# Performance work log

Hardware: AMD Instinct MI355X
Metric: run time of the kernel (lower is better)

## Reference

```python
import jax, jax.numpy as jnp
import numpy as np

V, E, H, L, T, B = 50257, 1024, 16, 12, 128, 16
FF = 4 * E
STD = 0.02


def setup_inputs() -> dict:
    key = jax.random.key(0)
    ks = jax.random.split(key, 20)
    n = lambda k, shape: (jax.random.normal(k, shape, dtype=jnp.float32) * STD)
    inp = {
        'idx': jax.random.randint(ks[0], (B, T), 0, V, dtype=jnp.int64),
        'targets': jax.random.randint(ks[1], (B, T), 0, V, dtype=jnp.int64),
        'tok_emb': n(ks[2], (V, E)),
        'pos_emb': n(ks[3], (T, E)),
        'wq': n(ks[4], (L, E, E)),
        'wk': n(ks[5], (L, E, E)),
        'wv': n(ks[6], (L, E, E)),
        'w_proj': n(ks[7], (L, E, E)),
        'b_proj': jnp.zeros((L, E), jnp.float32),
        'ln1_g': jnp.ones((L, E), jnp.float32),
        'ln1_b': jnp.zeros((L, E), jnp.float32),
        'ln2_g': jnp.ones((L, E), jnp.float32),
        'ln2_b': jnp.zeros((L, E), jnp.float32),
        'w_fc1': n(ks[8], (L, E, FF)),
        'b_fc1': jnp.zeros((L, FF), jnp.float32),
        'w_fc2': n(ks[9], (L, FF, E)),
        'b_fc2': jnp.zeros((L, E), jnp.float32),
        'lnf_g': jnp.ones((E,), jnp.float32),
        'lnf_b': jnp.zeros((E,), jnp.float32),
        'w_head': n(ks[10], (E, V)),
        'b_head': jnp.zeros((V,), jnp.float32),
    }
    return inp


def _layernorm(x, g, b, eps=1e-5):
    m = x.mean(-1, keepdims=True)
    v = ((x - m) ** 2).mean(-1, keepdims=True)
    return (x - m) / jnp.sqrt(v + eps) * g + b


def _forward(idx, targets, tok_emb, pos_emb, wq, wk, wv, w_proj, b_proj,
             ln1_g, ln1_b, ln2_g, ln2_b, w_fc1, b_fc1, w_fc2, b_fc2,
             lnf_g, lnf_b, w_head, b_head):
    Bb, Tt = idx.shape
    x = tok_emb[idx] + pos_emb[:Tt]  # (B, T, E)
    causal = jnp.tril(jnp.ones((Tt, Tt), dtype=bool))
    scale = E ** (-0.5)  # NOTE: original scales by full n_embd, not head_size

    def block(x, p):
        (wq_l, wk_l, wv_l, wp_l, bp_l, g1, b1, g2, b2, wf1, bf1, wf2, bf2) = p
        h = _layernorm(x, g1, b1)
        q = (h @ wq_l).reshape(Bb, Tt, H, -1)
        k = (h @ wk_l).reshape(Bb, Tt, H, -1)
        v = (h @ wv_l).reshape(Bb, Tt, H, -1)
        sc = jnp.einsum('bthd,bshd->bhts', q, k) * scale
        sc = jnp.where(causal, sc, -jnp.inf)
        att = jax.nn.softmax(sc, axis=-1)
        o = jnp.einsum('bhts,bshd->bthd', att, v).reshape(Bb, Tt, E)
        x = x + o @ wp_l + bp_l
        h2 = _layernorm(x, g2, b2)
        x = x + jax.nn.relu(h2 @ wf1 + bf1) @ wf2 + bf2
        return x, None

    x, _ = jax.lax.scan(block, x, (wq, wk, wv, w_proj, b_proj, ln1_g, ln1_b,
                                   ln2_g, ln2_b, w_fc1, b_fc1, w_fc2, b_fc2))
    x = _layernorm(x, lnf_g, lnf_b)
    logits = x @ w_head + b_head  # (B, T, V)
    logp = jax.nn.log_softmax(logits, axis=-1)
    nll = -jnp.take_along_axis(logp.reshape(Bb * Tt, -1),
                               targets.reshape(-1, 1), axis=1)
    loss = nll.mean()
    return logits, loss


def reference(idx, targets, tok_emb, pos_emb, wq, wk, wv, w_proj, b_proj,
              ln1_g, ln1_b, ln2_g, ln2_b, w_fc1, b_fc1, w_fc2, b_fc2,
              lnf_g, lnf_b, w_head, b_head):
    return _forward(idx, targets, tok_emb, pos_emb, wq, wk, wv, w_proj, b_proj,
                    ln1_g, ln1_b, ln2_g, ln2_b, w_fc1, b_fc1, w_fc2, b_fc2,
                    lnf_g, lnf_b, w_head, b_head)
```

## Files before the change

kernel.cpp:

```cpp
#include <hip/hip_runtime.h>
#include <math.h>

typedef unsigned short u16;
typedef float f32x4 __attribute__((ext_vector_type(4)));
typedef short bf16x8 __attribute__((ext_vector_type(8)));
typedef unsigned short us4 __attribute__((ext_vector_type(4)));

#define DEVI __device__ __forceinline__

DEVI float bf2f(u16 u) { return __uint_as_float(((unsigned int)u) << 16); }
DEVI u16 f2bf(float f) {
    unsigned int u = __float_as_uint(f);
    u += 0x7fffu + ((u >> 16) & 1u);
    return (u16)(u >> 16);
}

__global__ __launch_bounds__(256) void k_embed(const int* __restrict__ idx,
                                               const float* __restrict__ te,
                                               const float* __restrict__ pe,
                                               float* __restrict__ x) {
    int m = blockIdx.x;
    int t = m & 127;
    int tok = idx[m];
    const f32x4* a = (const f32x4*)(te + (long)tok * 1024);
    const f32x4* p = (const f32x4*)(pe + (long)t * 1024);
    f32x4* o = (f32x4*)(x + (long)m * 1024);
    o[threadIdx.x] = a[threadIdx.x] + p[threadIdx.x];
}

DEVI void ln_body(f32x4 v, const float* g, const float* b, float* red,
                  int tid, int lane, int wid, u16* outrow) {
    float s = v.x + v.y + v.z + v.w;
#pragma unroll
    for (int o2 = 32; o2; o2 >>= 1) s += __shfl_xor(s, o2);
    if (lane == 0) red[wid] = s;
    __syncthreads();
    float mean = (red[0] + red[1] + red[2] + red[3]) * (1.0f / 1024.0f);
    f32x4 d; d.x = v.x - mean; d.y = v.y - mean; d.z = v.z - mean; d.w = v.w - mean;
    float sq = d.x * d.x + d.y * d.y + d.z * d.z + d.w * d.w;
#pragma unroll
    for (int o2 = 32; o2; o2 >>= 1) sq += __shfl_xor(sq, o2);
    if (lane == 0) red[4 + wid] = sq;
    __syncthreads();
    float rstd = rsqrtf((red[4] + red[5] + red[6] + red[7]) * (1.0f / 1024.0f) + 1e-5f);
    f32x4 gg = ((const f32x4*)g)[tid];
    f32x4 bb = ((const f32x4*)b)[tid];
    us4 o4;
    o4.x = f2bf(d.x * rstd * gg.x + bb.x);
    o4.y = f2bf(d.y * rstd * gg.y + bb.y);
    o4.z = f2bf(d.z * rstd * gg.z + bb.z);
    o4.w = f2bf(d.w * rstd * gg.w + bb.w);
    ((us4*)outrow)[tid] = o4;
}

__global__ __launch_bounds__(256) void k_ln(const float* __restrict__ x,
                                            const float* __restrict__ g,
                                            const float* __restrict__ b,
                                            u16* __restrict__ out) {
    __shared__ float red[8];
    int tid = threadIdx.x, lane = tid & 63, wid = tid >> 6;
    int r = blockIdx.x;
    f32x4 v = ((const f32x4*)(x + (long)r * 1024))[tid];
    ln_body(v, g, b, red, tid, lane, wid, out + (long)r * 1024);
}

__global__ __launch_bounds__(256) void k_comb_ln(float* __restrict__ x,
                                                 const float* __restrict__ p01,
                                                 const float* __restrict__ bias,
                                                 const float* __restrict__ g,
                                                 const float* __restrict__ b,
                                                 u16* __restrict__ out) {
    __shared__ float red[8];
    int tid = threadIdx.x, lane = tid & 63, wid = tid >> 6;
    int r = blockIdx.x;
    f32x4 v = ((const f32x4*)(x + (long)r * 1024))[tid];
    f32x4 p0 = ((const f32x4*)(p01 + (long)r * 1024))[tid];
    f32x4 p1 = ((const f32x4*)(p01 + 2048L * 1024 + (long)r * 1024))[tid];
    f32x4 bv = ((const f32x4*)bias)[tid];
    v.x += p0.x + p1.x + bv.x; v.y += p0.y + p1.y + bv.y;
    v.z += p0.z + p1.z + bv.z; v.w += p0.w + p1.w + bv.w;
    ((f32x4*)(x + (long)r * 1024))[tid] = v;
    ln_body(v, g, b, red, tid, lane, wid, out + (long)r * 1024);
}

DEVI void tr_tile(const float* __restrict__ in, u16* __restrict__ out,
                  int K, int N, int k0, int n0, int tid, float (*tile)[65]) {
    int trow = tid >> 4;
    int tcol = (tid & 15) * 4;
#pragma unroll
    for (int p = 0; p < 4; ++p) {
        int k = k0 + trow + p * 16;
        const float* src = in + (long)k * N + n0 + tcol;
#pragma unroll
        for (int j = 0; j < 4; ++j) {
            int n = n0 + tcol + j;
            tile[trow + p * 16][tcol + j] = (n < N) ? src[j] : 0.0f;
        }
    }
    __syncthreads();
#pragma unroll
    for (int p = 0; p < 4; ++p) {
        int n = n0 + trow + p * 16;
        if (n < N) {
            us4 o4;
#pragma unroll
            for (int j = 0; j < 4; ++j) o4[j] = f2bf(tile[tcol + j][trow + p * 16]);
            *(us4*)(out + (long)n * K + k0 + tcol) = o4;
        }
    }
}

__global__ __launch_bounds__(256) void k_tr_one(const float* __restrict__ in,
                                                u16* __restrict__ out, int K, int N) {
    __shared__ float tile[64][65];
    tr_tile(in, out, K, N, blockIdx.y * 64, blockIdx.x * 64, threadIdx.x, tile);
}

__global__ __launch_bounds__(256) void k_tr_layer(
    const float* __restrict__ wq, const float* __restrict__ wk,
    const float* __restrict__ wv, const float* __restrict__ wp,
    const float* __restrict__ f1, const float* __restrict__ f2,
    u16* __restrict__ oqkv, u16* __restrict__ oproj,
    u16* __restrict__ of1, u16* __restrict__ of2) {
    __shared__ float tile[64][65];
    int id = blockIdx.x;
    const float* in; u16* out; int K, N, txx, tyy;
    if (id < 1024) {
        int t = id >> 8, s2 = id & 255;
        txx = s2 & 15; tyy = s2 >> 4; K = 1024; N = 1024;
        in = (t == 0) ? wq : (t == 1) ? wk : (t == 2) ? wv : wp;
        out = (t == 3) ? oproj : oqkv + (long)t * 1024 * 1024;
    } else if (id < 2048) {
        int s2 = id - 1024;
        txx = s2 & 63; tyy = s2 >> 6; K = 1024; N = 4096; in = f1; out = of1;
    } else {
        int s2 = id - 2048;
        txx = s2 & 15; tyy = s2 >> 4; K = 4096; N = 1024; in = f2; out = of2;
    }
    tr_tile(in, out, K, N, tyy * 64, txx * 64, threadIdx.x, tile);
}

template <int ROWS>
DEVI void stage_tile(const u16* __restrict__ g, long row0, long rowmax, int ld,
                     int col0, char* lds, int tid) {
    constexpr int NCH = ROWS * 8;
#pragma unroll
    for (int p = 0; p < NCH / 256; ++p) {
        int c = tid + p * 256;
        int row = c >> 3;
        int gslot = c & 7;
        int gdata = gslot ^ (row & 7);
        long gr = row0 + row;
        if (gr > rowmax) gr = rowmax;
        const u16* src = g + gr * (long)ld + col0 + gdata * 8;
        char* dst = lds + ((long)((tid & 192) + p * 256)) * 16;
        __builtin_amdgcn_global_load_lds(
            (const __attribute__((address_space(1))) void*)src,
            (__attribute__((address_space(3))) void*)dst, 16, 0, 0);
    }
}

template <int ROWS>
DEVI void stage32(const u16* __restrict__ g, long row0, long rowmax, int ld,
                  int col0, char* lds, int tid) {
    constexpr int NP = ROWS * 4 / 512;
#pragma unroll
    for (int p = 0; p < NP; ++p) {
        int c = tid + p * 512;
        int row = c >> 2;
        int gslot = c & 3;
        int gdata = gslot ^ (row & 3) ^ ((row >> 2) & 3);
        long gr = row0 + row;
        if (gr > rowmax) gr = rowmax;
        const u16* src = g + gr * (long)ld + col0 + gdata * 8;
        char* dst = lds + ((long)((tid & 448) + p * 512)) * 16;
        __builtin_amdgcn_global_load_lds(
            (const __attribute__((address_space(1))) void*)src,
            (__attribute__((address_space(3))) void*)dst, 16, 0, 0);
    }
}

template <int BN, bool OUT_BF16, bool RELU, bool HAS_BIAS, bool HAS_RES, bool SPLITK>
__global__ __launch_bounds__(256, 2) void k_gemm(
    const u16* __restrict__ A, const u16* __restrict__ Bt,
    const float* __restrict__ bias, const float* __restrict__ res,
    float* __restrict__ Cf, u16* __restrict__ Cb,
    int M, int N, int K, int ldk, int ldc) {
    constexpr int NR = BN / 32;
    constexpr int ASZ = 128 * 64 * 2;
    constexpr int BSZ = BN * 64 * 2;
    __shared__ __align__(16) char lds[2 * (ASZ + BSZ)];
    int tid = threadIdx.x, lane = tid & 63, wid = tid >> 6;
    int l15 = lane & 15, l4 = lane >> 4;
    int wr = wid >> 1, wc = wid & 1;
    if constexpr (SPLITK) {
        int h = blockIdx.z;
        A += (long)h * K;
        Bt += (long)h * K;
        Cf += (long)h * M * (long)ldc;
    }
    long m0 = (long)blockIdx.y * 128;
    long n0 = (long)blockIdx.x * BN;
    f32x4 acc[4][NR] = {};
    const int nk = K >> 6;

    stage_tile<128>(A, m0, (long)M - 1, ldk, 0, lds, tid);
    stage_tile<BN>(Bt, n0, (long)N - 1, ldk, 0, lds + ASZ, tid);
    int cur = 0;
    for (int kt = 0; kt < nk; ++kt) {
        __syncthreads();
        if (kt + 1 < nk) {
            char* nb = lds + (cur ^ 1) * (ASZ + BSZ);
            stage_tile<128>(A, m0, (long)M - 1, ldk, (kt + 1) << 6, nb, tid);
            stage_tile<BN>(Bt, n0, (long)N - 1, ldk, (kt + 1) << 6, nb + ASZ, tid);
        }
        const char* ab = lds + cur * (ASZ + BSZ);
        const char* bb = ab + ASZ;
#pragma unroll
        for (int kh = 0; kh < 2; ++kh) {
            bf16x8 af[4], bfv[NR];
#pragma unroll
            for (int mi = 0; mi < 4; ++mi) {
                int row = wr * 64 + mi * 16 + l15;
                int slot = (kh * 4 + l4) ^ (row & 7);
                af[mi] = *(const bf16x8*)(ab + (row * 8 + slot) * 16);
            }
#pragma unroll
            for (int ni = 0; ni < NR; ++ni) {
                int row = wc * (BN / 2) + ni * 16 + l15;
                int slot = (kh * 4 + l4) ^ (row & 7);
                bfv[ni] = *(const bf16x8*)(bb + (row * 8 + slot) * 16);
            }
#pragma unroll
            for (int mi = 0; mi < 4; ++mi)
#pragma unroll
                for (int ni = 0; ni < NR; ++ni)
                    acc[mi][ni] = __builtin_amdgcn_mfma_f32_16x16x32_bf16(
                        af[mi], bfv[ni], acc[mi][ni], 0, 0, 0);
        }
        cur ^= 1;
    }
#pragma unroll
    for (int ni = 0; ni < NR; ++ni) {
        long n = n0 + wc * (BN / 2) + ni * 16 + l15;
        if (n < N) {
            float bv = HAS_BIAS ? bias[n] : 0.0f;
#pragma unroll
            for (int mi = 0; mi < 4; ++mi) {
#pragma unroll
                for (int j = 0; j < 4; ++j) {
                    long m = m0 + wr * 64 + mi * 16 + l4 * 4 + j;
                    float v = acc[mi][ni][j] + bv;
                    if (HAS_RES) v += res[m * (long)ldc + n];
                    if (RELU) v = fmaxf(v, 0.0f);
                    if (OUT_BF16) Cb[m * (long)ldc + n] = f2bf(v);
                    else Cf[m * (long)ldc + n] = v;
                }
            }
        }
    }
}

__global__ __launch_bounds__(512, 4) void k_head256(
    const u16* __restrict__ A, const u16* __restrict__ Bt,
    const float* __restrict__ bias, float* __restrict__ Cf,
    float2* __restrict__ part, int M, int N, int K, int ldc) {
    constexpr int ASZ = 256 * 32 * 2;
    constexpr int BSZ = 128 * 32 * 2;
    constexpr int TSZ = ASZ + BSZ;
    __shared__ __align__(16) char lds[128 * 129 * 4];
    int tid = threadIdx.x, lane = tid & 63, wid = tid >> 6;
    int l15 = lane & 15, l4 = lane >> 4;
    int wr = wid >> 1, wc = wid & 1;
    int bn = blockIdx.x, bm = blockIdx.y;
    long m0 = (long)bm * 256, n0 = (long)bn * 128;
    f32x4 acc[4][4] = {};
    const int nk = K >> 5;

    stage32<256>(A, m0, (long)M - 1, K, 0, lds, tid);
    stage32<128>(Bt, n0, (long)N - 1, K, 0, lds + ASZ, tid);
    int cur = 0;
    for (int kt = 0; kt < nk; ++kt) {
        __syncthreads();
        if (kt + 1 < nk) {
            char* nb = lds + (cur ^ 1) * TSZ;
            stage32<256>(A, m0, (long)M - 1, K, (kt + 1) << 5, nb, tid);
            stage32<128>(Bt, n0, (long)N - 1, K, (kt + 1) << 5, nb + ASZ, tid);
        }
        const char* ab = lds + cur * TSZ;
        const char* bb = ab + ASZ;
        bf16x8 af[4], bfv[4];
#pragma unroll
        for (int mi = 0; mi < 4; ++mi) {
            int row = wr * 64 + mi * 16 + l15;
            int slot = (l4 ^ (row & 3) ^ ((row >> 2) & 3)) & 3;
            af[mi] = *(const bf16x8*)(ab + (row * 4 + slot) * 16);
        }
#pragma unroll
        for (int ni = 0; ni < 4; ++ni) {
            int row = wc * 64 + ni * 16 + l15;
            int slot = (l4 ^ (row & 3) ^ ((row >> 2) & 3)) & 3;
            bfv[ni] = *(const bf16x8*)(bb + (row * 4 + slot) * 16);
        }
#pragma unroll
        for (int mi = 0; mi < 4; ++mi)
#pragma unroll
            for (int ni = 0; ni < 4; ++ni)
                acc[mi][ni] = __builtin_amdgcn_mfma_f32_16x16x32_bf16(
                    af[mi], bfv[ni], acc[mi][ni], 0, 0, 0);
        cur ^= 1;
    }
    const float BIG_NEG = -1e30f;
    float bvv[4];
#pragma unroll
    for (int ni = 0; ni < 4; ++ni) {
        long n = n0 + wc * 64 + ni * 16 + l15;
        bvv[ni] = (n < N) ? bias[n] : 0.0f;
    }
    float* ldsF = (float*)lds;
#pragma unroll
    for (int pass = 0; pass < 2; ++pass) {
        int rbase = pass * 128;
        __syncthreads();
        if ((wr >> 1) == pass) {
#pragma unroll
            for (int mi = 0; mi < 4; ++mi)
#pragma unroll
                for (int ni = 0; ni < 4; ++ni)
#pragma unroll
                    for (int j = 0; j < 4; ++j) {
                        int row = wr * 64 + mi * 16 + l4 * 4 + j - rbase;
                        int col = wc * 64 + ni * 16 + l15;
                        long n = n0 + col;
                        float v = acc[mi][ni][j] + bvv[ni];
                        if (n >= N) v = BIG_NEG;
                        ldsF[row * 129 + col] = v;
                    }
        }
        __syncthreads();
#pragma unroll 4
        for (int i = 0; i < 32; ++i) {
            int flat = tid + (i << 9);
            int row = flat >> 7, col = flat & 127;
            long n = n0 + col;
            if (n < N)
                __builtin_nontemporal_store(ldsF[row * 129 + col],
                                            &Cf[(m0 + rbase + row) * (long)ldc + n]);
        }
        if (tid < 256) {
            int r = tid >> 1, half = tid & 1;
            const float* rp = ldsF + r * 129 + half * 64;
            float mx = BIG_NEG;
#pragma unroll 8
            for (int c = 0; c < 64; ++c) mx = fmaxf(mx, rp[c]);
            float sm = 0.f;
#pragma unroll 8
            for (int c = 0; c < 64; ++c) sm += __expf(rp[c] - mx);
            float mo = __shfl_xor(mx, 1), so = __shfl_xor(sm, 1);
            float nm = fmaxf(mx, mo);
            float S = sm * __expf(mx - nm) + so * __expf(mo - nm);
            if (half == 0)
                part[(long)bn * M + m0 + rbase + r] = make_float2(nm, S);
        }
    }
}

__global__ __launch_bounds__(256) void k_attn_mfma(const u16* __restrict__ qkv,
                                                   u16* __restrict__ o) {
    __shared__ __align__(16) u16 Ks[128 * 64];
    __shared__ __align__(16) u16 Vt[64 * 128];
    __shared__ __align__(16) u16 Ps[4][32 * 128];
    int tid = threadIdx.x, lane = tid & 63, w = tid >> 6;
    int l15 = lane & 15, l4 = lane >> 4;
    int b = blockIdx.x >> 4, h = blockIdx.x & 15;
    const u16* base = qkv + (long)b * 128 * 3072 + h * 64;

    stage_tile<128>(base + 1024, 0, 127, 3072, 0, (char*)Ks, tid);
    {
        const u16* vg = base + 2048;
#pragma unroll
        for (int p = 0; p < 4; ++p) {
            int s0 = (w * 4 + p) * 8;
            u16 tmp[8];
#pragma unroll
            for (int j = 0; j < 8; ++j) tmp[j] = vg[(long)(s0 + j) * 3072 + lane];
            int slot = (s0 >> 3) ^ (lane & 7);
            *(bf16x8*)((char*)Vt + lane * 256 + slot * 16) = *(bf16x8*)tmp;
        }
    }
    bf16x8 aq[2][2];
#pragma unroll
    for (int mj = 0; mj < 2; ++mj)
#pragma unroll
        for (int kk = 0; kk < 2; ++kk)
            aq[mj][kk] = *(const bf16x8*)(base + (long)(w * 32 + mj * 16 + l15) * 3072 + kk * 32 + l4 * 8);
    __syncthreads();

    f32x4 sacc[2][8] = {};
#pragma unroll
    for (int sj = 0; sj < 8; ++sj) {
        bf16x8 bk[2];
#pragma unroll
        for (int kk = 0; kk < 2; ++kk) {
            int row = sj * 16 + l15;
            int slot = (kk * 4 + l4) ^ (row & 7);
            bk[kk] = *(const bf16x8*)((char*)Ks + (row * 8 + slot) * 16);
        }
#pragma unroll
        for (int mj = 0; mj < 2; ++mj) {
            sacc[mj][sj] = __builtin_amdgcn_mfma_f32_16x16x32_bf16(aq[mj][0], bk[0], sacc[mj][sj], 0, 0, 0);
            sacc[mj][sj] = __builtin_amdgcn_mfma_f32_16x16x32_bf16(aq[mj][1], bk[1], sacc[mj][sj], 0, 0, 0);
        }
    }
    const float scale = 0.03125f;
#pragma unroll
    for (int mj = 0; mj < 2; ++mj) {
#pragma unroll
        for (int j = 0; j < 4; ++j) {
            int tq = w * 32 + mj * 16 + l4 * 4 + j;
            float mx = -INFINITY;
#pragma unroll
            for (int sj = 0; sj < 8; ++sj) {
                int s = sj * 16 + l15;
                float v = (s <= tq) ? sacc[mj][sj][j] * scale : -INFINITY;
                sacc[mj][sj][j] = v;
                mx = fmaxf(mx, v);
            }
#pragma unroll
            for (int ofs = 1; ofs < 16; ofs <<= 1) mx = fmaxf(mx, __shfl_xor(mx, ofs));
            float sm = 0.f;
#pragma unroll
            for (int sj = 0; sj < 8; ++sj) {
                float e = __expf(sacc[mj][sj][j] - mx);
                sacc[mj][sj][j] = e;
                sm += e;
            }
#pragma unroll
            for (int ofs = 1; ofs < 16; ofs <<= 1) sm += __shfl_xor(sm, ofs);
            float inv = 1.0f / sm;
            int m2 = mj * 16 + l4 * 4 + j;
            u16* prow = Ps[w] + m2 * 128;
#pragma unroll
            for (int sj = 0; sj < 8; ++sj) {
                int s = sj * 16 + l15;
                int slot = (s >> 3) ^ (m2 & 7);
                prow[slot * 8 + (s & 7)] = f2bf(sacc[mj][sj][j] * inv);
            }
        }
    }
    f32x4 oacc[2][4] = {};
#pragma unroll
    for (int kk = 0; kk < 4; ++kk) {
        bf16x8 pa[2], bv[4];
#pragma unroll
        for (int mj = 0; mj < 2; ++mj) {
            int m2 = mj * 16 + l15;
            int slot = (kk * 4 + l4) ^ (m2 & 7);
            pa[mj] = *(const bf16x8*)((char*)(Ps[w]) + m2 * 256 + slot * 16);
        }
#pragma unroll
        for (int nb = 0; nb < 4; ++nb) {
            int d = nb * 16 + l15;
            int slot = (kk * 4 + l4) ^ (d & 7);
            bv[nb] = *(const bf16x8*)((char*)Vt + d * 256 + slot * 16);
        }
#pragma unroll
        for (int mj = 0; mj < 2; ++mj)
#pragma unroll
            for (int nb = 0; nb < 4; ++nb)
                oacc[mj][nb] = __builtin_amdgcn_mfma_f32_16x16x32_bf16(pa[mj], bv[nb], oacc[mj][nb], 0, 0, 0);
    }
#pragma unroll
    for (int mj = 0; mj < 2; ++mj)
#pragma unroll
        for (int nb = 0; nb < 4; ++nb) {
            int d = nb * 16 + l15;
#pragma unroll
            for (int j = 0; j < 4; ++j) {
                int tq = w * 32 + mj * 16 + l4 * 4 + j;
                o[((long)b * 128 + tq) * 1024 + h * 64 + d] = f2bf(oacc[mj][nb][j]);
            }
        }
}

__global__ __launch_bounds__(64) void k_loss_rows2(const float2* __restrict__ part,
                                                   const float* __restrict__ logits,
                                                   const int* __restrict__ tgt,
                                                   float* __restrict__ rowloss, int ncb) {
    int r = blockIdx.x, lane = threadIdx.x;
    float M = -1e30f, S = 0.f;
    for (int cb = lane; cb < ncb; cb += 64) {
        float2 p = part[(long)cb * 2048 + r];
        float nm = fmaxf(M, p.x);
        S = S * __expf(M - nm) + p.y * __expf(p.x - nm);
        M = nm;
    }
#pragma unroll
    for (int ofs = 32; ofs; ofs >>= 1) {
        float M2 = __shfl_xor(M, ofs), S2 = __shfl_xor(S, ofs);
        float nm = fmaxf(M, M2);
        S = S * __expf(M - nm) + S2 * __expf(M2 - nm);
        M = nm;
    }
    if (lane == 0)
        rowloss[r] = (M + logf(S)) - logits[(long)r * 50257 + tgt[r]];
}

__global__ __launch_bounds__(256) void k_loss_reduce(const float* __restrict__ rowloss,
                                                     float* __restrict__ out) {
    __shared__ float red[4];
    int tid = threadIdx.x, lane = tid & 63, wid = tid >> 6;
    float s = 0.f;
    for (int i = tid; i < 2048; i += 256) s += rowloss[i];
#pragma unroll
    for (int ofs = 32; ofs; ofs >>= 1) s += __shfl_xor(s, ofs);
    if (lane == 0) red[wid] = s;
    __syncthreads();
    if (tid == 0) out[0] = (red[0] + red[1] + red[2] + red[3]) * (1.0f / 2048.0f);
}

extern "C" void kernel_launch(void* const* d_in, const int* in_sizes, int n_in,
                              void* d_out, int out_size, void* d_ws, size_t ws_size,
                              hipStream_t stream) {
    (void)in_sizes; (void)n_in; (void)out_size; (void)ws_size;
    const int*   idx     = (const int*)d_in[0];
    const int*   targets = (const int*)d_in[1];
    const float* tok_emb = (const float*)d_in[2];
    const float* pos_emb = (const float*)d_in[3];
    const float* wq      = (const float*)d_in[4];
    const float* wk      = (const float*)d_in[5];
    const float* wv      = (const float*)d_in[6];
    const float* w_proj  = (const float*)d_in[7];
    const float* b_proj  = (const float*)d_in[8];
    const float* ln1_g   = (const float*)d_in[9];
    const float* ln1_b   = (const float*)d_in[10];
    const float* ln2_g   = (const float*)d_in[11];
    const float* ln2_b   = (const float*)d_in[12];
    const float* w_fc1   = (const float*)d_in[13];
    const float* b_fc1   = (const float*)d_in[14];
    const float* w_fc2   = (const float*)d_in[15];
    const float* b_fc2   = (const float*)d_in[16];
    const float* lnf_g   = (const float*)d_in[17];
    const float* lnf_b   = (const float*)d_in[18];
    const float* w_head  = (const float*)d_in[19];
    const float* b_head  = (const float*)d_in[20];
    float* out = (float*)d_out;

    char* w = (char*)d_ws;
    auto alloc = [&](size_t bytes) {
        char* p = w;
        w += (bytes + 255) & ~(size_t)255;
        return p;
    };
    u16*    wT_qkv  = (u16*)alloc(3072L * 1024 * 2);
    u16*    wT_proj = (u16*)alloc(1024L * 1024 * 2);
    u16*    wT_f1   = (u16*)alloc(4096L * 1024 * 2);
    u16*    wT_f2   = (u16*)alloc(1024L * 4096 * 2);
    u16*    wT_head = (u16*)alloc(50257L * 1024 * 2);
    float*  x       = (float*)alloc(2048L * 1024 * 4);
    u16*    h_bf    = (u16*)alloc(2048L * 1024 * 2);
    u16*    qkvb    = (u16*)alloc(2048L * 3072 * 2);
    u16*    o_bf    = (u16*)alloc(2048L * 1024 * 2);
    u16*    ff_bf   = (u16*)alloc(2048L * 4096 * 2);
    float*  p01     = (float*)alloc(2L * 2048 * 1024 * 4);
    float2* part    = (float2*)alloc(393L * 2048 * 8);
    float*  rowloss = (float*)alloc(2048L * 4);

    k_embed<<<2048, 256, 0, stream>>>(idx, tok_emb, pos_emb, x);
    k_tr_one<<<dim3(786, 16), 256, 0, stream>>>(w_head, wT_head, 1024, 50257);

    for (int l = 0; l < 12; ++l) {
        k_tr_layer<<<3072, 256, 0, stream>>>(
            wq + (long)l * 1048576, wk + (long)l * 1048576,
            wv + (long)l * 1048576, w_proj + (long)l * 1048576,
            w_fc1 + (long)l * 4194304, w_fc2 + (long)l * 4194304,
            wT_qkv, wT_proj, wT_f1, wT_f2);
        if (l == 0)
            k_ln<<<2048, 256, 0, stream>>>(x, ln1_g, ln1_b, h_bf);
        else
            k_comb_ln<<<2048, 256, 0, stream>>>(x, p01, b_fc2 + (l - 1) * 1024,
                                                ln1_g + l * 1024, ln1_b + l * 1024, h_bf);
        k_gemm<128, true, false, false, false, false><<<dim3(24, 16), 256, 0, stream>>>(
            h_bf, wT_qkv, nullptr, nullptr, nullptr, qkvb, 2048, 3072, 1024, 1024, 3072);
        k_attn_mfma<<<256, 256, 0, stream>>>(qkvb, o_bf);
        k_gemm<64, false, false, false, false, true><<<dim3(16, 16, 2), 256, 0, stream>>>(
            o_bf, wT_proj, nullptr, nullptr, p01, nullptr, 2048, 1024, 512, 1024, 1024);
        k_comb_ln<<<2048, 256, 0, stream>>>(x, p01, b_proj + l * 1024,
                                            ln2_g + l * 1024, ln2_b + l * 1024, h_bf);
        k_gemm<128, true, true, true, false, false><<<dim3(32, 16), 256, 0, stream>>>(
            h_bf, wT_f1, b_fc1 + l * 4096, nullptr, nullptr, ff_bf, 2048, 4096, 1024, 1024, 4096);
        k_gemm<64, false, false, false, false, true><<<dim3(16, 16, 2), 256, 0, stream>>>(
            ff_bf, wT_f2, nullptr, nullptr, p01, nullptr, 2048, 1024, 2048, 4096, 1024);
    }
    k_comb_ln<<<2048, 256, 0, stream>>>(x, p01, b_fc2 + 11 * 1024, lnf_g, lnf_b, h_bf);
    k_head256<<<dim3(393, 8), 512, 0, stream>>>(h_bf, wT_head, b_head, out, part,
                                                2048, 50257, 1024, 50257);
    k_loss_rows2<<<2048, 64, 0, stream>>>(part, out, targets, rowloss, 393);
    k_loss_reduce<<<1, 256, 0, stream>>>(rowloss, out + 102926336L);
}
```

Measured before the change: 1.856 ms.

## Retile LM head GEMM to 256x64 tiles with 256 threads and BK=64

```diff
diff --git a/kernel.cpp b/kernel.cpp
--- a/kernel.cpp
+++ b/kernel.cpp
@@ -160,26 +160,6 @@
     }
 }
 
-template <int ROWS>
-DEVI void stage32(const u16* __restrict__ g, long row0, long rowmax, int ld,
-                  int col0, char* lds, int tid) {
-    constexpr int NP = ROWS * 4 / 512;
-#pragma unroll
-    for (int p = 0; p < NP; ++p) {
-        int c = tid + p * 512;
-        int row = c >> 2;
-        int gslot = c & 3;
-        int gdata = gslot ^ (row & 3) ^ ((row >> 2) & 3);
-        long gr = row0 + row;
-        if (gr > rowmax) gr = rowmax;
-        const u16* src = g + gr * (long)ld + col0 + gdata * 8;
-        char* dst = lds + ((long)((tid & 448) + p * 512)) * 16;
-        __builtin_amdgcn_global_load_lds(
-            (const __attribute__((address_space(1))) void*)src,
-            (__attribute__((address_space(3))) void*)dst, 16, 0, 0);
-    }
-}
-
 template <int BN, bool OUT_BF16, bool RELU, bool HAS_BIAS, bool HAS_RES, bool SPLITK>
 __global__ __launch_bounds__(256, 2) void k_gemm(
     const u16* __restrict__ A, const u16* __restrict__ Bt,
@@ -261,107 +241,98 @@
     }
 }
 
-__global__ __launch_bounds__(512, 4) void k_head256(
+__global__ __launch_bounds__(256, 2) void k_head(
     const u16* __restrict__ A, const u16* __restrict__ Bt,
     const float* __restrict__ bias, float* __restrict__ Cf,
     float2* __restrict__ part, int M, int N, int K, int ldc) {
-    constexpr int ASZ = 256 * 32 * 2;
-    constexpr int BSZ = 128 * 32 * 2;
+    constexpr int ASZ = 256 * 64 * 2;
+    constexpr int BSZ = 64 * 64 * 2;
     constexpr int TSZ = ASZ + BSZ;
-    __shared__ __align__(16) char lds[128 * 129 * 4];
+    __shared__ __align__(16) char lds[2 * TSZ];
     int tid = threadIdx.x, lane = tid & 63, wid = tid >> 6;
     int l15 = lane & 15, l4 = lane >> 4;
-    int wr = wid >> 1, wc = wid & 1;
     int bn = blockIdx.x, bm = blockIdx.y;
-    long m0 = (long)bm * 256, n0 = (long)bn * 128;
+    long m0 = (long)bm * 256, n0 = (long)bn * 64;
     f32x4 acc[4][4] = {};
-    const int nk = K >> 5;
-
-    stage32<256>(A, m0, (long)M - 1, K, 0, lds, tid);
-    stage32<128>(Bt, n0, (long)N - 1, K, 0, lds + ASZ, tid);
+    const int nk = K >> 6;
+
+    stage_tile<256>(A, m0, (long)M - 1, K, 0, lds, tid);
+    stage_tile<64>(Bt, n0, (long)N - 1, K, 0, lds + ASZ, tid);
     int cur = 0;
     for (int kt = 0; kt < nk; ++kt) {
         __syncthreads();
         if (kt + 1 < nk) {
             char* nb = lds + (cur ^ 1) * TSZ;
-            stage32<256>(A, m0, (long)M - 1, K, (kt + 1) << 5, nb, tid);
-            stage32<128>(Bt, n0, (long)N - 1, K, (kt + 1) << 5, nb + ASZ, tid);
+            stage_tile<256>(A, m0, (long)M - 1, K, (kt + 1) << 6, nb, tid);
+            stage_tile<64>(Bt, n0, (long)N - 1, K, (kt + 1) << 6, nb + ASZ, tid);
         }
         const char* ab = lds + cur * TSZ;
         const char* bb = ab + ASZ;
-        bf16x8 af[4], bfv[4];
-#pragma unroll
-        for (int mi = 0; mi < 4; ++mi) {
-            int row = wr * 64 + mi * 16 + l15;
-            int slot = (l4 ^ (row & 3) ^ ((row >> 2) & 3)) & 3;
-            af[mi] = *(const bf16x8*)(ab + (row * 4 + slot) * 16);
-        }
-#pragma unroll
-        for (int ni = 0; ni < 4; ++ni) {
-            int row = wc * 64 + ni * 16 + l15;
-            int slot = (l4 ^ (row & 3) ^ ((row >> 2) & 3)) & 3;
-            bfv[ni] = *(const bf16x8*)(bb + (row * 4 + slot) * 16);
-        }
-#pragma unroll
-        for (int mi = 0; mi < 4; ++mi)
-#pragma unroll
-            for (int ni = 0; ni < 4; ++ni)
-                acc[mi][ni] = __builtin_amdgcn_mfma_f32_16x16x32_bf16(
-                    af[mi], bfv[ni], acc[mi][ni], 0, 0, 0);
+#pragma unroll
+        for (int kh = 0; kh < 2; ++kh) {
+            bf16x8 af[4], bfv[4];
+#pragma unroll
+            for (int mi = 0; mi < 4; ++mi) {
+                int row = wid * 64 + mi * 16 + l15;
+                int slot = (kh * 4 + l4) ^ (row & 7);
+                af[mi] = *(const bf16x8*)(ab + (row * 8 + slot) * 16);
+            }
+#pragma unroll
+            for (int ni = 0; ni < 4; ++ni) {
+                int row = ni * 16 + l15;
+                int slot = (kh * 4 + l4) ^ (row & 7);
+                bfv[ni] = *(const bf16x8*)(bb + (row * 8 + slot) * 16);
+            }
+#pragma unroll
+            for (int mi = 0; mi < 4; ++mi)
+#pragma unroll
+                for (int ni = 0; ni < 4; ++ni)
+                    acc[mi][ni] = __builtin_amdgcn_mfma_f32_16x16x32_bf16(
+                        af[mi], bfv[ni], acc[mi][ni], 0, 0, 0);
+        }
         cur ^= 1;
     }
     const float BIG_NEG = -1e30f;
     float bvv[4];
 #pragma unroll
     for (int ni = 0; ni < 4; ++ni) {
-        long n = n0 + wc * 64 + ni * 16 + l15;
+        long n = n0 + ni * 16 + l15;
         bvv[ni] = (n < N) ? bias[n] : 0.0f;
     }
+    __syncthreads();
     float* ldsF = (float*)lds;
 #pragma unroll
-    for (int pass = 0; pass < 2; ++pass) {
-        int rbase = pass * 128;
-        __syncthreads();
-        if ((wr >> 1) == pass) {
-#pragma unroll
-            for (int mi = 0; mi < 4; ++mi)
-#pragma unroll
-                for (int ni = 0; ni < 4; ++ni)
-#pragma unroll
-                    for (int j = 0; j < 4; ++j) {
-                        int row = wr * 64 + mi * 16 + l4 * 4 + j - rbase;
-                        int col = wc * 64 + ni * 16 + l15;
-                        long n = n0 + col;
-                        float v = acc[mi][ni][j] + bvv[ni];
-                        if (n >= N) v = BIG_NEG;
-                        ldsF[row * 129 + col] = v;
-                    }
-        }
-        __syncthreads();
+    for (int mi = 0; mi < 4; ++mi)
+#pragma unroll
+        for (int ni = 0; ni < 4; ++ni)
+#pragma unroll
+            for (int j = 0; j < 4; ++j) {
+                int row = wid * 64 + mi * 16 + l4 * 4 + j;
+                int col = ni * 16 + l15;
+                long n = n0 + col;
+                float v = acc[mi][ni][j] + bvv[ni];
+                if (n >= N) v = BIG_NEG;
+                ldsF[row * 65 + col] = v;
+            }
+    __syncthreads();
 #pragma unroll 4
-        for (int i = 0; i < 32; ++i) {
-            int flat = tid + (i << 9);
-            int row = flat >> 7, col = flat & 127;
-            long n = n0 + col;
-            if (n < N)
-                __builtin_nontemporal_store(ldsF[row * 129 + col],
-                                            &Cf[(m0 + rbase + row) * (long)ldc + n]);
-        }
-        if (tid < 256) {
-            int r = tid >> 1, half = tid & 1;
-            const float* rp = ldsF + r * 129 + half * 64;
-            float mx = BIG_NEG;
+    for (int i = 0; i < 64; ++i) {
+        int flat = tid + (i << 8);
+        int row = flat >> 6, col = flat & 63;
+        long n = n0 + col;
+        if (n < N)
+            __builtin_nontemporal_store(ldsF[row * 65 + col],
+                                        &Cf[(m0 + row) * (long)ldc + n]);
+    }
+    {
+        const float* rp = ldsF + tid * 65;
+        float mx = BIG_NEG;
 #pragma unroll 8
-            for (int c = 0; c < 64; ++c) mx = fmaxf(mx, rp[c]);
-            float sm = 0.f;
+        for (int c = 0; c < 64; ++c) mx = fmaxf(mx, rp[c]);
+        float sm = 0.f;
 #pragma unroll 8
-            for (int c = 0; c < 64; ++c) sm += __expf(rp[c] - mx);
-            float mo = __shfl_xor(mx, 1), so = __shfl_xor(sm, 1);
-            float nm = fmaxf(mx, mo);
-            float S = sm * __expf(mx - nm) + so * __expf(mo - nm);
-            if (half == 0)
-                part[(long)bn * M + m0 + rbase + r] = make_float2(nm, S);
-        }
+        for (int c = 0; c < 64; ++c) sm += __expf(rp[c] - mx);
+        part[(long)bn * M + m0 + tid] = make_float2(mx, sm);
     }
 }
 
@@ -563,7 +534,7 @@
     u16*    o_bf    = (u16*)alloc(2048L * 1024 * 2);
     u16*    ff_bf   = (u16*)alloc(2048L * 4096 * 2);
     float*  p01     = (float*)alloc(2L * 2048 * 1024 * 4);
-    float2* part    = (float2*)alloc(393L * 2048 * 8);
+    float2* part    = (float2*)alloc(786L * 2048 * 8);
     float*  rowloss = (float*)alloc(2048L * 4);
 
     k_embed<<<2048, 256, 0, stream>>>(idx, tok_emb, pos_emb, x);
@@ -593,8 +564,8 @@
             ff_bf, wT_f2, nullptr, nullptr, p01, nullptr, 2048, 1024, 2048, 4096, 1024);
     }
     k_comb_ln<<<2048, 256, 0, stream>>>(x, p01, b_fc2 + 11 * 1024, lnf_g, lnf_b, h_bf);
-    k_head256<<<dim3(393, 8), 512, 0, stream>>>(h_bf, wT_head, b_head, out, part,
-                                                2048, 50257, 1024, 50257);
-    k_loss_rows2<<<2048, 64, 0, stream>>>(part, out, targets, rowloss, 393);
+    k_head<<<dim3(786, 8), 256, 0, stream>>>(h_bf, wT_head, b_head, out, part,
+                                             2048, 50257, 1024, 50257);
+    k_loss_rows2<<<2048, 64, 0, stream>>>(part, out, targets, rowloss, 786);
     k_loss_reduce<<<1, 256, 0, stream>>>(rowloss, out + 102926336L);
 }
```

Result: no change. 1.878 ms (+1.2%).
